# Kernel optimization log

Measured on AMD Instinct MI355X. Metric: run time of the kernel, lower is better.

The kernel has to match this reference:

```python
import jax, jax.numpy as jnp
import numpy as np
from functools import partial

D_MODEL = 1024
D_STATE = 128
D_INNER = 2 * D_MODEL          # 2048
HEADS = D_MODEL                # dt width == d_model -> one dt per head
HEAD_DIM = D_INNER // HEADS    # 2
KERNEL = 4
PROJ_OUT = 2 * D_INNER + 2 * D_STATE + D_MODEL  # 5376


def setup_inputs() -> dict:
    key = jax.random.key(0)
    ks = jax.random.split(key, 8)
    B, L = 2, 2048
    u = jax.random.normal(ks[0], (B, L, D_MODEL), dtype=jnp.float32)
    W_in = jax.random.normal(ks[1], (D_MODEL, PROJ_OUT), dtype=jnp.float32) * 0.02
    conv_w = jax.random.normal(ks[2], (D_INNER, 1, KERNEL), dtype=jnp.float32) * 0.2
    conv_b = jnp.zeros((D_INNER,), dtype=jnp.float32)
    W_out = jax.random.normal(ks[3], (D_INNER, D_MODEL), dtype=jnp.float32) * 0.02
    ln_g = jnp.ones((D_MODEL,), dtype=jnp.float32)
    ln_b = jnp.zeros((D_MODEL,), dtype=jnp.float32)
    A_log = jnp.log(jax.random.uniform(ks[4], (HEADS,), minval=1.0, maxval=16.0)).astype(jnp.float32)
    return {"u": u, "W_in": W_in, "conv_w": conv_w, "conv_b": conv_b,
            "W_out": W_out, "ln_g": ln_g, "ln_b": ln_b, "A_log": A_log}


def _layernorm(x, g, b, eps=1e-5):
    mu = jnp.mean(x, axis=-1, keepdims=True)
    var = jnp.var(x, axis=-1, keepdims=True)
    return (x - mu) * jax.lax.rsqrt(var + eps) * g + b


def _mamba2_forward(u, W_in, conv_w, conv_b, W_out, ln_g, ln_b, A_log):
    B, L, _ = u.shape
    xn = _layernorm(u, ln_g, ln_b)
    zxbcdt = xn @ W_in                                   # (B, L, PROJ_OUT)
    x, z, Bc, Cc, dt = jnp.split(
        zxbcdt, [D_INNER, 2 * D_INNER, 2 * D_INNER + D_STATE,
                 2 * D_INNER + 2 * D_STATE], axis=-1)
    # causal depthwise conv over time (pad left KERNEL-1)
    xc = jnp.transpose(x, (0, 2, 1))                     # (B, C, L)
    xc = jnp.pad(xc, ((0, 0), (0, 0), (KERNEL - 1, 0)))
    xc = jax.lax.conv_general_dilated(
        xc, conv_w, window_strides=(1,), padding='VALID',
        dimension_numbers=('NCH', 'OIH', 'NCH'),
        feature_group_count=D_INNER) + conv_b[None, :, None]
    x = jax.nn.silu(jnp.transpose(xc, (0, 2, 1)))        # (B, L, d_inner)

    dt = jax.nn.softplus(dt)                             # (B, L, H)
    A = -jnp.exp(A_log)                                  # (H,)
    decay = jnp.exp(dt * A)                              # (B, L, H)
    xh = x.reshape(B, L, HEADS, HEAD_DIM)                # (B, L, H, P)

    # time-major for scan
    def step(h, inp):
        dec_t, dt_t, x_t, B_t, C_t = inp                 # (B,H),(B,H),(B,H,P),(B,N),(B,N)
        h = dec_t[..., None, None] * h + \
            (dt_t[..., None] * x_t)[..., None] * B_t[:, None, None, :]
        y_t = jnp.einsum('bhpn,bn->bhp', h, C_t)
        return h, y_t

    tm = lambda a: jnp.swapaxes(a, 0, 1)
    h0 = jnp.zeros((B, HEADS, HEAD_DIM, D_STATE), dtype=u.dtype)
    _, ys = jax.lax.scan(step, h0, (tm(decay), tm(dt), tm(xh), tm(Bc), tm(Cc)))
    y = jnp.swapaxes(ys, 0, 1).reshape(B, L, D_INNER)    # (B, L, d_inner)

    y = y * jax.nn.silu(z)
    return u + y @ W_out                                 # residual


def reference(u, W_in, conv_w, conv_b, W_out, ln_g, ln_b, A_log):
    return _mamba2_forward(u, W_in, conv_w, conv_b, W_out, ln_g, ln_b, A_log)
```

## Files before the change

kernel.cpp:

```cpp
#include <hip/hip_runtime.h>
#include <hip/hip_bf16.h>
#include <stdint.h>

typedef __bf16 bf16_t;
typedef bf16_t bf16x8 __attribute__((ext_vector_type(8)));
typedef bf16_t bf16x4 __attribute__((ext_vector_type(4)));
typedef bf16_t bf16x2 __attribute__((ext_vector_type(2)));
typedef float  f32x4  __attribute__((ext_vector_type(4)));

#define D_MODEL 1024
#define D_STATE 128
#define D_INNER 2048
#define HEADS   1024
#define PROJ    5376
#define LSEQ    2048
#define BATCH   2
#define NROW    (BATCH*LSEQ)
#define QCH     64
#define NC      (LSEQ/QCH)

#define OFF_X   0
#define OFF_Z   2048
#define OFF_B   4096
#define OFF_C   4224
#define OFF_DT  4352

#define LOG2E 1.44269504088896340736f

typedef __attribute__((address_space(1))) void void_as1;
typedef __attribute__((address_space(3))) void void_as3;

__device__ __forceinline__ void gload_lds16(const void* g, void* l) {
  __builtin_amdgcn_global_load_lds((void_as1*)(uintptr_t)g,
                                   (void_as3*)(uint32_t)(uintptr_t)l,
                                   16, 0, 0);
}

__device__ __forceinline__ float siluf(float v) { return v / (1.f + expf(-v)); }

__device__ __forceinline__ float exp2_fast(float x) {
  float r;
  asm("v_exp_f32 %0, %1" : "=v"(r) : "v"(x));
  return r;
}

__device__ __forceinline__ float rdlane(float v, int l) {
  return __int_as_float(__builtin_amdgcn_readlane(__float_as_int(v), l));
}

template<int CTRL, int RM>
__device__ __forceinline__ float dpp_add(float x) {
  int s = __builtin_amdgcn_update_dpp(0, __float_as_int(x), CTRL, RM, 0xf, true);
  return x + __int_as_float(s);
}

__global__ __launch_bounds__(256) void transpose_kernel(const float* __restrict__ src,
                                                        bf16_t* __restrict__ dst,
                                                        int R, int C) {
  __shared__ float tile[32][33];
  int c0 = blockIdx.x * 32, r0 = blockIdx.y * 32;
  int tx = threadIdx.x, ty = threadIdx.y;
  #pragma unroll
  for (int i = ty; i < 32; i += 8)
    tile[i][tx] = src[(size_t)(r0 + i) * C + c0 + tx];
  __syncthreads();
  #pragma unroll
  for (int i = ty; i < 32; i += 8)
    dst[(size_t)(c0 + i) * R + r0 + tx] = (bf16_t)tile[tx][i];
}

__global__ __launch_bounds__(256) void ln_kernel(const float* __restrict__ u,
                                                 const float* __restrict__ g,
                                                 const float* __restrict__ bb,
                                                 bf16_t* __restrict__ xn) {
  int row = blockIdx.x;
  int t = threadIdx.x;
  float4 v = ((const float4*)(u + (size_t)row * D_MODEL))[t];
  float s  = v.x + v.y + v.z + v.w;
  float s2 = v.x*v.x + v.y*v.y + v.z*v.z + v.w*v.w;
  #pragma unroll
  for (int m = 1; m < 64; m <<= 1) { s += __shfl_xor(s, m, 64); s2 += __shfl_xor(s2, m, 64); }
  __shared__ float ws[8];
  int wv = t >> 6, lane = t & 63;
  if (lane == 0) { ws[wv] = s; ws[4 + wv] = s2; }
  __syncthreads();
  s  = ws[0] + ws[1] + ws[2] + ws[3];
  s2 = ws[4] + ws[5] + ws[6] + ws[7];
  float mean = s * (1.f / D_MODEL);
  float var  = s2 * (1.f / D_MODEL) - mean * mean;
  float rstd = rsqrtf(var + 1e-5f);
  float4 gv = ((const float4*)g)[t];
  float4 bv = ((const float4*)bb)[t];
  bf16x4 o;
  o[0] = (bf16_t)((v.x - mean) * rstd * gv.x + bv.x);
  o[1] = (bf16_t)((v.y - mean) * rstd * gv.y + bv.y);
  o[2] = (bf16_t)((v.z - mean) * rstd * gv.z + bv.z);
  o[3] = (bf16_t)((v.w - mean) * rstd * gv.w + bv.w);
  *(bf16x4*)(xn + (size_t)row * D_MODEL + t * 4) = o;
}

template<typename CT>
__global__ __launch_bounds__(256) void gemm_bt(const bf16_t* __restrict__ A,
                                               const bf16_t* __restrict__ BT,
                                               CT* __restrict__ C,
                                               int M, int N, int K,
                                               const float* __restrict__ resid,
                                               int tilesPerBatch,
                                               long long sA, long long sB, long long sC) {
  __shared__ bf16_t lA[128 * 32];
  __shared__ bf16_t lB[128 * 32];
  int bat = blockIdx.x / tilesPerBatch;
  int tl  = blockIdx.x % tilesPerBatch;
  A += (size_t)bat * sA; BT += (size_t)bat * sB; C += (size_t)bat * sC;
  int ntile = N >> 7;
  int tm = tl / ntile, tn = tl % ntile;
  int m0 = tm << 7, n0 = tn << 7;
  int t = threadIdx.x;
  int wv = t >> 6, lane = t & 63;
  int wm = (wv >> 1) << 6, wn = (wv & 1) << 6;
  int l15 = lane & 15, l4 = lane >> 4;

  f32x4 acc[4][4];
  #pragma unroll
  for (int i = 0; i < 4; ++i)
    #pragma unroll
    for (int j = 0; j < 4; ++j) acc[i][j] = (f32x4){0.f, 0.f, 0.f, 0.f};

  int sr = t >> 2;
  int sk = (t & 3) * 8;
  const bf16_t* ga  = A  + (size_t)(m0 + sr) * K + sk;
  const bf16_t* ga2 = ga + (size_t)64 * K;
  const bf16_t* gb  = BT + (size_t)(n0 + sr) * K + sk;
  const bf16_t* gb2 = gb + (size_t)64 * K;
  bf16_t* la  = lA + t * 8;
  bf16_t* la2 = la + 2048;
  bf16_t* lb  = lB + t * 8;
  bf16_t* lb2 = lb + 2048;

  const bf16_t* raBase = lA + (wm + l15) * 32 + l4 * 8;
  const bf16_t* rbBase = lB + (wn + l15) * 32 + l4 * 8;

  for (int k0 = 0; k0 < K; k0 += 32) {
    gload_lds16(ga, la);  gload_lds16(ga2, la2);
    gload_lds16(gb, lb);  gload_lds16(gb2, lb2);
    ga += 32; ga2 += 32; gb += 32; gb2 += 32;
    __syncthreads();
    bf16x8 af[4], bq[4];
    #pragma unroll
    for (int f = 0; f < 4; ++f) {
      af[f] = *(const bf16x8*)(raBase + f * 512);
      bq[f] = *(const bf16x8*)(rbBase + f * 512);
    }
    #pragma unroll
    for (int i = 0; i < 4; ++i)
      #pragma unroll
      for (int j = 0; j < 4; ++j)
        acc[i][j] = __builtin_amdgcn_mfma_f32_16x16x32_bf16(af[i], bq[j], acc[i][j], 0, 0, 0);
    __syncthreads();
  }

  #pragma unroll
  for (int i = 0; i < 4; ++i) {
    int row = m0 + wm + i * 16 + l4 * 4;
    #pragma unroll
    for (int j = 0; j < 4; ++j) {
      int col = n0 + wn + j * 16 + l15;
      #pragma unroll
      for (int r = 0; r < 4; ++r) {
        size_t idx = (size_t)(row + r) * N + col;
        float v = acc[i][j][r];
        if (resid) v += resid[idx];
        C[idx] = (CT)v;
      }
    }
  }
}

__global__ __launch_bounds__(256) void prep_kernel(const bf16_t* __restrict__ zxb,
                                                   const float* __restrict__ conv_w,
                                                   const float* __restrict__ conv_b,
                                                   const float* __restrict__ A_log,
                                                   float* __restrict__ dta,
                                                   bf16_t* __restrict__ dtx) {
  int idx = blockIdx.x * 256 + threadIdx.x;
  int h  = idx & (HEADS - 1);
  int bt = idx >> 10;
  int t  = bt & (LSEQ - 1);
  float draw = (float)zxb[(size_t)bt * PROJ + OFF_DT + h];
  float dt = (draw > 20.f) ? draw : log1pf(expf(draw));
  float Ah = -expf(A_log[h]);
  dta[idx] = dt * Ah;
  float4 w0 = *(const float4*)(conv_w + 8 * h);
  float4 w1 = *(const float4*)(conv_w + 8 * h + 4);
  float2 cb = *(const float2*)(conv_b + 2 * h);
  float acc0 = cb.x, acc1 = cb.y;
  float w0a[4] = {w0.x, w0.y, w0.z, w0.w};
  float w1a[4] = {w1.x, w1.y, w1.z, w1.w};
  #pragma unroll
  for (int k = 0; k < 4; ++k) {
    int tt = t - 3 + k;
    if (tt >= 0) {
      bf16x2 xv = *(const bf16x2*)(zxb + (size_t)(bt - 3 + k) * PROJ + OFF_X + 2 * h);
      acc0 = fmaf((float)xv[0], w0a[k], acc0);
      acc1 = fmaf((float)xv[1], w1a[k], acc1);
    }
  }
  float xs0 = siluf(acc0), xs1 = siluf(acc1);
  bf16x2 o; o[0] = (bf16_t)(dt * xs0); o[1] = (bf16_t)(dt * xs1);
  *(bf16x2*)(dtx + 2 * (size_t)idx) = o;
}

__global__ __launch_bounds__(256) void kg_kernel(const bf16_t* __restrict__ zxb,
                                                 float* __restrict__ GT,
                                                 bf16_t* __restrict__ BTc) {
  __shared__ bf16_t lB[QCH * 128];
  __shared__ bf16_t lC[QCH * 128];
  int bc = blockIdx.x;
  int b = bc / NC, c = bc % NC;
  int t = threadIdx.x;
  size_t rowbase = ((size_t)b * LSEQ + c * QCH);
  #pragma unroll
  for (int p = 0; p < 4; ++p) {
    int row = p * 16 + (t >> 4);
    int eo  = (t & 15) * 8;
    gload_lds16(zxb + (rowbase + row) * PROJ + OFF_B + eo, lB + p * 2048 + t * 8);
    gload_lds16(zxb + (rowbase + row) * PROJ + OFF_C + eo, lC + p * 2048 + t * 8);
  }
  __syncthreads();
  int wv = t >> 6, lane = t & 63;
  int l15 = lane & 15, l4 = lane >> 4;
  f32x4 acc[4];
  #pragma unroll
  for (int i = 0; i < 4; ++i) acc[i] = (f32x4){0.f, 0.f, 0.f, 0.f};
  #pragma unroll
  for (int ks = 0; ks < 4; ++ks) {
    bf16x8 af = *(const bf16x8*)(lB + (16 * wv + l15) * 128 + ks * 32 + l4 * 8);
    #pragma unroll
    for (int it = 0; it < 4; ++it) {
      bf16x8 bq = *(const bf16x8*)(lC + (16 * it + l15) * 128 + ks * 32 + l4 * 8);
      acc[it] = __builtin_amdgcn_mfma_f32_16x16x32_bf16(af, bq, acc[it], 0, 0, 0);
    }
  }
  float* gout = GT + (size_t)bc * 4096;
  #pragma unroll
  for (int it = 0; it < 4; ++it) {
    int col = it * 16 + l15;
    #pragma unroll
    for (int r = 0; r < 4; ++r) {
      int j = 16 * wv + l4 * 4 + r;
      gout[j * 64 + col] = acc[it][r];
    }
  }
  bf16_t* bto = BTc + (size_t)bc * (128 * QCH);
  int n = t >> 1, j0 = (t & 1) * 32;
  #pragma unroll
  for (int jj = 0; jj < 32; ++jj)
    bto[n * QCH + j0 + jj] = lB[(j0 + jj) * 128 + n];
}

__global__ __launch_bounds__(512) void local_kernel(const float* __restrict__ GT,
                                                    const float* __restrict__ dta,
                                                    const bf16_t* __restrict__ dtx,
                                                    float* __restrict__ y,
                                                    bf16_t* __restrict__ S,
                                                    bf16_t* __restrict__ cdb,
                                                    float* __restrict__ Dch) {
  __shared__ float sp[4096];
  __shared__ float sy[QCH * 17];
  int t = threadIdx.x;
  int wv = t >> 6, l = t & 63;
  int hg = blockIdx.x & 127;
  int c  = (blockIdx.x >> 7) & (NC - 1);
  int b  = blockIdx.x >> 12;
  int bc = b * NC + c;
  int h  = hg * 8 + wv;

  {
    const float* gsrc = GT + (size_t)bc * 4096 + t * 8;
    float4 a = *(const float4*)gsrc;
    float4 bq = *(const float4*)(gsrc + 4);
    int j  = t >> 3;
    int i0 = (t & 7) * 8;
    float va[8] = {a.x, a.y, a.z, a.w, bq.x, bq.y, bq.z, bq.w};
    float* dstb = sp + (j >> 1) * 128 + (j & 1);
    #pragma unroll
    for (int k = 0; k < 8; ++k) {
      int i = i0 + k;
      dstb[i * 2] = (j <= i) ? va[k] : 0.f;
    }
  }

  int tIdx = c * QCH + l;
  size_t bt = (size_t)b * LSEQ + tIdx;
  float dtal = dta[bt * HEADS + h];
  bf16x2 vvb = *(const bf16x2*)(dtx + bt * D_INNER + 2 * h);
  float v0 = (float)vvb[0], v1 = (float)vvb[1];

  float ca = dtal;
  ca = dpp_add<0x111, 0xf>(ca);
  ca = dpp_add<0x112, 0xf>(ca);
  ca = dpp_add<0x114, 0xf>(ca);
  ca = dpp_add<0x118, 0xf>(ca);
  ca = dpp_add<0x142, 0xa>(ca);
  ca = dpp_add<0x143, 0xc>(ca);
  float ca2 = ca * LOG2E;

  float cdl = exp2_fast(ca2);
  cdb[((size_t)b * HEADS + h) * LSEQ + tIdx] = (bf16_t)cdl;
  float calast2 = rdlane(ca2, 63);
  float sc = exp2_fast(calast2 - ca2);
  bf16_t* srow = S + ((size_t)bc * D_INNER + 2 * h) * QCH + l;
  srow[0]   = (bf16_t)(sc * v0);
  srow[QCH] = (bf16_t)(sc * v1);
  if (l == 63) Dch[((size_t)b * HEADS + h) * NC + c] = cdl;
  __syncthreads();

  float y0 = 0.f, y1 = 0.f;
  const float* spb = sp + l * 2;
  #pragma unroll
  for (int j2 = 0; j2 < 32; ++j2) {
    float2 g2 = *(const float2*)(spb + j2 * 128);
    {
      float cj2 = rdlane(ca2, 2 * j2);
      float sv0 = rdlane(v0, 2 * j2);
      float sv1 = rdlane(v1, 2 * j2);
      float e = exp2_fast(fminf(ca2 - cj2, 0.f));
      float gg = e * g2.x;
      y0 = fmaf(gg, sv0, y0);
      y1 = fmaf(gg, sv1, y1);
    }
    {
      float cj2 = rdlane(ca2, 2 * j2 + 1);
      float sv0 = rdlane(v0, 2 * j2 + 1);
      float sv1 = rdlane(v1, 2 * j2 + 1);
      float e = exp2_fast(fminf(ca2 - cj2, 0.f));
      float gg = e * g2.y;
      y0 = fmaf(gg, sv0, y0);
      y1 = fmaf(gg, sv1, y1);
    }
  }
  sy[l * 17 + wv * 2]     = y0;
  sy[l * 17 + wv * 2 + 1] = y1;
  __syncthreads();
  int rowt = t >> 3, cc = (t & 7) * 2;
  float2 o = make_float2(sy[rowt * 17 + cc], sy[rowt * 17 + cc + 1]);
  *(float2*)(y + ((size_t)b * LSEQ + c * QCH + rowt) * D_INNER + hg * 16 + cc) = o;
}

__global__ __launch_bounds__(256) void state_kernel(bf16_t* __restrict__ Hst,
                                                    const float* __restrict__ Dch) {
  int g = blockIdx.x * 256 + threadIdx.x;
  int nq = g & 31;
  int hp = (g >> 5) & (D_INNER - 1);
  int b  = g >> 16;
  int h  = hp >> 1;
  const float* Dp = Dch + ((size_t)b * HEADS + h) * NC;
  float4 cur = make_float4(0.f, 0.f, 0.f, 0.f);
  for (int c = 0; c < NC; ++c) {
    size_t idx = (((size_t)(b * NC + c) * D_INNER) + hp) * D_STATE + nq * 4;
    bf16x4 old = *(bf16x4*)(Hst + idx);
    bf16x4 w;
    w[0] = (bf16_t)cur.x; w[1] = (bf16_t)cur.y; w[2] = (bf16_t)cur.z; w[3] = (bf16_t)cur.w;
    *(bf16x4*)(Hst + idx) = w;
    float d = Dp[c];
    cur.x = fmaf(d, cur.x, (float)old[0]);
    cur.y = fmaf(d, cur.y, (float)old[1]);
    cur.z = fmaf(d, cur.z, (float)old[2]);
    cur.w = fmaf(d, cur.w, (float)old[3]);
  }
}

__global__ __launch_bounds__(256) void ycross_kernel(const bf16_t* __restrict__ zxb,
                                                     const bf16_t* __restrict__ Hst,
                                                     const bf16_t* __restrict__ cdb,
                                                     float* __restrict__ y) {
  __shared__ bf16_t lA[QCH * 32];
  __shared__ bf16_t lB[256 * 32];
  int nt = blockIdx.x & 7;
  int c  = (blockIdx.x >> 3) & (NC - 1);
  int b  = blockIdx.x >> 8;
  int bc = b * NC + c;
  int n0 = nt * 256;
  int t = threadIdx.x;
  int wv = t >> 6, lane = t & 63;
  int l15 = lane & 15, l4 = lane >> 4;
  size_t rowbase = (size_t)b * LSEQ + c * QCH;

  f32x4 acc[4][4];
  #pragma unroll
  for (int i = 0; i < 4; ++i)
    #pragma unroll
    for (int j = 0; j < 4; ++j) acc[i][j] = (f32x4){0.f, 0.f, 0.f, 0.f};

  int sr = t >> 2, sk = (t & 3) * 8;
  for (int ks = 0; ks < 4; ++ks) {
    int k0 = ks * 32;
    gload_lds16(zxb + (rowbase + sr) * PROJ + OFF_C + k0 + sk, lA + t * 8);
    #pragma unroll
    for (int p = 0; p < 4; ++p)
      gload_lds16(Hst + ((size_t)bc * D_INNER + n0 + p * 64 + sr) * D_STATE + k0 + sk,
                  lB + p * 2048 + t * 8);
    __syncthreads();
    #pragma unroll
    for (int i = 0; i < 4; ++i) {
      bf16x8 af = *(const bf16x8*)(lA + (i * 16 + l15) * 32 + l4 * 8);
      #pragma unroll
      for (int j = 0; j < 4; ++j) {
        bf16x8 bq = *(const bf16x8*)(lB + (wv * 64 + j * 16 + l15) * 32 + l4 * 8);
        acc[i][j] = __builtin_amdgcn_mfma_f32_16x16x32_bf16(af, bq, acc[i][j], 0, 0, 0);
      }
    }
    __syncthreads();
  }

  #pragma unroll
  for (int i = 0; i < 4; ++i) {
    int row = i * 16 + l4 * 4;
    #pragma unroll
    for (int j = 0; j < 4; ++j) {
      int col = n0 + wv * 64 + j * 16 + l15;
      int h = col >> 1;
      bf16x4 cd4 = *(const bf16x4*)(cdb + ((size_t)b * HEADS + h) * LSEQ + c * QCH + row);
      #pragma unroll
      for (int r = 0; r < 4; ++r) {
        size_t idx = (rowbase + row + r) * D_INNER + col;
        y[idx] += (float)cd4[r] * acc[i][j][r];
      }
    }
  }
}

__global__ __launch_bounds__(256) void gate_kernel(const float* __restrict__ y,
                                                   const bf16_t* __restrict__ zxb,
                                                   bf16_t* __restrict__ yg) {
  int tid = blockIdx.x * 256 + threadIdx.x;
  int row = tid >> 9;
  int c0  = (tid & 511) * 4;
  float4 yv = *(const float4*)(y + (size_t)row * D_INNER + c0);
  bf16x4 zv = *(const bf16x4*)(zxb + (size_t)row * PROJ + OFF_Z + c0);
  bf16x4 o;
  o[0] = (bf16_t)(yv.x * siluf((float)zv[0]));
  o[1] = (bf16_t)(yv.y * siluf((float)zv[1]));
  o[2] = (bf16_t)(yv.z * siluf((float)zv[2]));
  o[3] = (bf16_t)(yv.w * siluf((float)zv[3]));
  *(bf16x4*)(yg + (size_t)row * D_INNER + c0) = o;
}

extern "C" void kernel_launch(void* const* d_in, const int* in_sizes, int n_in,
                              void* d_out, int out_size, void* d_ws, size_t ws_size,
                              hipStream_t stream) {
  const float* u      = (const float*)d_in[0];
  const float* W_in   = (const float*)d_in[1];
  const float* conv_w = (const float*)d_in[2];
  const float* conv_b = (const float*)d_in[3];
  const float* W_out  = (const float*)d_in[4];
  const float* ln_g   = (const float*)d_in[5];
  const float* ln_b   = (const float*)d_in[6];
  const float* A_log  = (const float*)d_in[7];
  float* out = (float*)d_out;

  char* ws = (char*)d_ws;
  bf16_t* W_inT  = (bf16_t*)ws;  ws += (size_t)PROJ * D_MODEL * 2;
  bf16_t* W_outT = (bf16_t*)ws;  ws += (size_t)D_MODEL * D_INNER * 2;
  bf16_t* xn     = (bf16_t*)ws;  ws += (size_t)NROW * D_MODEL * 2;
  bf16_t* zxb    = (bf16_t*)ws;  ws += (size_t)NROW * PROJ * 2;
  float*  dta    = (float*)ws;   ws += (size_t)NROW * HEADS * 4;
  bf16_t* dtx    = (bf16_t*)ws;  ws += (size_t)NROW * D_INNER * 2;
  float*  yy     = (float*)ws;   ws += (size_t)NROW * D_INNER * 4;
  bf16_t* yg     = (bf16_t*)ws;  ws += (size_t)NROW * D_INNER * 2;
  float*  GT     = (float*)ws;   ws += (size_t)BATCH * NC * 4096 * 4;
  bf16_t* BTc    = (bf16_t*)ws;  ws += (size_t)BATCH * NC * 128 * QCH * 2;
  bf16_t* S      = (bf16_t*)ws;  ws += (size_t)BATCH * NC * D_INNER * QCH * 2;
  bf16_t* cdb    = (bf16_t*)ws;  ws += (size_t)BATCH * HEADS * LSEQ * 2;
  float*  Dch    = (float*)ws;   ws += (size_t)BATCH * HEADS * NC * 4;
  bf16_t* Hst    = (bf16_t*)ws;  ws += (size_t)BATCH * NC * D_INNER * D_STATE * 2;

  dim3 tb(32, 8);
  transpose_kernel<<<dim3(PROJ / 32, D_MODEL / 32), tb, 0, stream>>>(W_in, W_inT, D_MODEL, PROJ);
  transpose_kernel<<<dim3(D_MODEL / 32, D_INNER / 32), tb, 0, stream>>>(W_out, W_outT, D_INNER, D_MODEL);
  ln_kernel<<<NROW, 256, 0, stream>>>(u, ln_g, ln_b, xn);
  gemm_bt<bf16_t><<<(NROW / 128) * (PROJ / 128), 256, 0, stream>>>(
      xn, W_inT, zxb, NROW, PROJ, D_MODEL, nullptr, (NROW / 128) * (PROJ / 128), 0, 0, 0);
  prep_kernel<<<NROW * HEADS / 256, 256, 0, stream>>>(zxb, conv_w, conv_b, A_log, dta, dtx);
  kg_kernel<<<BATCH * NC, 256, 0, stream>>>(zxb, GT, BTc);
  local_kernel<<<BATCH * NC * 128, 512, 0, stream>>>(GT, dta, dtx, yy, S, cdb, Dch);
  gemm_bt<bf16_t><<<BATCH * NC * 16, 256, 0, stream>>>(
      S, BTc, Hst, D_INNER, D_STATE, QCH, nullptr, 16,
      (long long)D_INNER * QCH, (long long)128 * QCH, (long long)D_INNER * D_STATE);
  state_kernel<<<BATCH * D_INNER * 32 / 256, 256, 0, stream>>>(Hst, Dch);
  ycross_kernel<<<BATCH * NC * 8, 256, 0, stream>>>(zxb, Hst, cdb, yy);
  gate_kernel<<<NROW * D_INNER / 4 / 256, 256, 0, stream>>>(yy, zxb, yg);
  gemm_bt<float><<<(NROW / 128) * (D_MODEL / 128), 256, 0, stream>>>(
      yg, W_outT, out, NROW, D_MODEL, D_INNER, u, (NROW / 128) * (D_MODEL / 128), 0, 0, 0);
}
```

Measured before the change: 412.2 us.

## Add pipelined 8-wave input-projection GEMM and double-buffer generic GEMM

```diff
diff --git a/kernel.cpp b/kernel.cpp
--- a/kernel.cpp
+++ b/kernel.cpp
@@ -99,6 +99,120 @@
   *(bf16x4*)(xn + (size_t)row * D_MODEL + t * 4) = o;
 }
 
+#define G1_NT 16
+#define MFMA_BF16(a,b,c) __builtin_amdgcn_mfma_f32_16x16x32_bf16(a,b,c,0,0,0)
+
+__global__ __launch_bounds__(512, 2) void gemm1_8ph(const bf16_t* __restrict__ A,
+                                                    const bf16_t* __restrict__ BT,
+                                                    bf16_t* __restrict__ C) {
+  __shared__ __align__(16) char smem[98304];
+  int bid = blockIdx.x;
+  int s8  = (bid & 7) * 84 + (bid >> 3);
+  int tm = s8 / 21, tn = s8 % 21;
+  int m0 = tm << 7, n0 = tn << 8;
+  int tid = threadIdx.x;
+  int wid = tid >> 6, lane = tid & 63;
+  int wm = wid >> 2, wn = wid & 3;
+  int l15 = lane & 15, l4 = lane >> 4;
+
+  const bf16_t* Ab = A  + (size_t)m0 * 1024;
+  const bf16_t* Bb = BT + (size_t)n0 * 1024;
+  int rowA = tid >> 3;
+  int gcol = ((tid & 7) ^ (rowA & 7)) * 8;
+
+  int sw0 = (l4 * 16) ^ ((l15 & 7) << 4);
+  int sw1 = sw0 ^ 64;
+  int ar0 = (wm * 32 + l15) * 128;
+  int ar1 = ar0 + 2048;
+  int br0 = (wn * 32 + l15) * 128;
+  int br1 = br0 + 2048;
+
+  f32x4 acc[2][2][2][2];
+  #pragma unroll
+  for (int a = 0; a < 2; ++a)
+    #pragma unroll
+    for (int b = 0; b < 2; ++b)
+      #pragma unroll
+      for (int c = 0; c < 2; ++c)
+        #pragma unroll
+        for (int d = 0; d < 2; ++d) acc[a][b][c][d] = (f32x4){0.f,0.f,0.f,0.f};
+
+#define STAGE_A(half, t) do { \
+    const bf16_t* _s = Ab + ((size_t)((half)*64 + rowA) * 1024) + (t)*64 + gcol; \
+    gload_lds16(_s, smem + ((t)&1)*49152 + (half)*8192 + tid*16); \
+  } while(0)
+#define STAGE_B(half, t) do { \
+    const bf16_t* _s = Bb + ((size_t)((half)*128 + rowA) * 1024) + (t)*64 + gcol; \
+    char* _d = smem + ((t)&1)*49152 + 16384 + (half)*16384 + tid*16; \
+    gload_lds16(_s, _d); \
+    gload_lds16(_s + 64*1024, _d + 8192); \
+  } while(0)
+
+#define PHASE(qm, qn, dd, STMT_STAGE, STMT_VM) do { \
+    const char* pa = smem + (dd)*49152 + (qm)*8192; \
+    const char* pb = smem + (dd)*49152 + 16384 + (qn)*16384; \
+    bf16x8 a00 = *(const bf16x8*)(pa + ar0 + sw0); \
+    bf16x8 a01 = *(const bf16x8*)(pa + ar0 + sw1); \
+    bf16x8 a10 = *(const bf16x8*)(pa + ar1 + sw0); \
+    bf16x8 a11 = *(const bf16x8*)(pa + ar1 + sw1); \
+    bf16x8 b00 = *(const bf16x8*)(pb + br0 + sw0); \
+    bf16x8 b01 = *(const bf16x8*)(pb + br0 + sw1); \
+    bf16x8 b10 = *(const bf16x8*)(pb + br1 + sw0); \
+    bf16x8 b11 = *(const bf16x8*)(pb + br1 + sw1); \
+    STMT_STAGE; \
+    __builtin_amdgcn_s_barrier(); \
+    asm volatile("s_waitcnt lgkmcnt(0)" ::: "memory"); \
+    __builtin_amdgcn_sched_barrier(0); \
+    __builtin_amdgcn_s_setprio(1); \
+    acc[qm][qn][0][0] = MFMA_BF16(a00, b00, acc[qm][qn][0][0]); \
+    acc[qm][qn][0][1] = MFMA_BF16(a00, b10, acc[qm][qn][0][1]); \
+    acc[qm][qn][1][0] = MFMA_BF16(a10, b00, acc[qm][qn][1][0]); \
+    acc[qm][qn][1][1] = MFMA_BF16(a10, b10, acc[qm][qn][1][1]); \
+    acc[qm][qn][0][0] = MFMA_BF16(a01, b01, acc[qm][qn][0][0]); \
+    acc[qm][qn][0][1] = MFMA_BF16(a01, b11, acc[qm][qn][0][1]); \
+    acc[qm][qn][1][0] = MFMA_BF16(a11, b01, acc[qm][qn][1][0]); \
+    acc[qm][qn][1][1] = MFMA_BF16(a11, b11, acc[qm][qn][1][1]); \
+    __builtin_amdgcn_s_setprio(0); \
+    __builtin_amdgcn_sched_barrier(0); \
+    STMT_VM; \
+    __builtin_amdgcn_s_barrier(); \
+  } while(0)
+
+  STAGE_A(0, 0); STAGE_B(0, 0); STAGE_B(1, 0); STAGE_A(1, 0);
+  STAGE_A(0, 1); STAGE_B(0, 1);
+  asm volatile("s_waitcnt vmcnt(3)" ::: "memory");
+  __builtin_amdgcn_s_barrier();
+
+  for (int t = 0; t < G1_NT; ++t) {
+    int dd = t & 1;
+    PHASE(0, 0, dd, { if (t + 1 < G1_NT) STAGE_B(1, t + 1); }, {});
+    PHASE(0, 1, dd, { if (t + 1 < G1_NT) STAGE_A(1, t + 1); }, {});
+    PHASE(1, 0, dd, { if (t + 2 < G1_NT) STAGE_A(0, t + 2); }, {});
+    PHASE(1, 1, dd, { if (t + 2 < G1_NT) STAGE_B(0, t + 2); },
+          { if (t <= G1_NT - 3) asm volatile("s_waitcnt vmcnt(3)" ::: "memory");
+            else                asm volatile("s_waitcnt vmcnt(0)" ::: "memory"); });
+  }
+
+  #pragma unroll
+  for (int qm = 0; qm < 2; ++qm)
+    #pragma unroll
+    for (int qn = 0; qn < 2; ++qn)
+      #pragma unroll
+      for (int mf = 0; mf < 2; ++mf)
+        #pragma unroll
+        for (int nf = 0; nf < 2; ++nf) {
+          int row = m0 + qm * 64 + wm * 32 + mf * 16 + l4 * 4;
+          int col = n0 + qn * 128 + wn * 32 + nf * 16 + l15;
+          f32x4 v = acc[qm][qn][mf][nf];
+          #pragma unroll
+          for (int r = 0; r < 4; ++r)
+            C[(size_t)(row + r) * PROJ + col] = (bf16_t)v[r];
+        }
+#undef STAGE_A
+#undef STAGE_B
+#undef PHASE
+}
+
 template<typename CT>
 __global__ __launch_bounds__(256) void gemm_bt(const bf16_t* __restrict__ A,
                                                const bf16_t* __restrict__ BT,
@@ -107,8 +221,8 @@
                                                const float* __restrict__ resid,
                                                int tilesPerBatch,
                                                long long sA, long long sB, long long sC) {
-  __shared__ bf16_t lA[128 * 32];
-  __shared__ bf16_t lB[128 * 32];
+  __shared__ __align__(16) bf16_t lA[2][128 * 32];
+  __shared__ __align__(16) bf16_t lB[2][128 * 32];
   int bat = blockIdx.x / tilesPerBatch;
   int tl  = blockIdx.x % tilesPerBatch;
   A += (size_t)bat * sA; BT += (size_t)bat * sB; C += (size_t)bat * sC;
@@ -132,32 +246,42 @@
   const bf16_t* ga2 = ga + (size_t)64 * K;
   const bf16_t* gb  = BT + (size_t)(n0 + sr) * K + sk;
   const bf16_t* gb2 = gb + (size_t)64 * K;
-  bf16_t* la  = lA + t * 8;
-  bf16_t* la2 = la + 2048;
-  bf16_t* lb  = lB + t * 8;
-  bf16_t* lb2 = lb + 2048;
-
-  const bf16_t* raBase = lA + (wm + l15) * 32 + l4 * 8;
-  const bf16_t* rbBase = lB + (wn + l15) * 32 + l4 * 8;
-
+
+  int raOff = (wm + l15) * 64 + l4 * 16;
+  int rbOff = (wn + l15) * 64 + l4 * 16;
+
+#define ST2(dd) do { \
+    char* _da = (char*)lA + (dd) * 8192 + t * 16; \
+    char* _db = (char*)lB + (dd) * 8192 + t * 16; \
+    gload_lds16(ga, _da);  gload_lds16(ga2, _da + 4096); \
+    gload_lds16(gb, _db);  gload_lds16(gb2, _db + 4096); \
+    ga += 32; ga2 += 32; gb += 32; gb2 += 32; \
+  } while(0)
+
+  ST2(0);
+  asm volatile("s_waitcnt vmcnt(0)" ::: "memory");
+  __builtin_amdgcn_s_barrier();
+
+  int cur = 0;
   for (int k0 = 0; k0 < K; k0 += 32) {
-    gload_lds16(ga, la);  gload_lds16(ga2, la2);
-    gload_lds16(gb, lb);  gload_lds16(gb2, lb2);
-    ga += 32; ga2 += 32; gb += 32; gb2 += 32;
-    __syncthreads();
+    if (k0 + 32 < K) ST2(cur ^ 1);
     bf16x8 af[4], bq[4];
     #pragma unroll
     for (int f = 0; f < 4; ++f) {
-      af[f] = *(const bf16x8*)(raBase + f * 512);
-      bq[f] = *(const bf16x8*)(rbBase + f * 512);
+      af[f] = *(const bf16x8*)((const char*)lA + cur * 8192 + raOff + f * 1024);
+      bq[f] = *(const bf16x8*)((const char*)lB + cur * 8192 + rbOff + f * 1024);
     }
     #pragma unroll
     for (int i = 0; i < 4; ++i)
       #pragma unroll
       for (int j = 0; j < 4; ++j)
-        acc[i][j] = __builtin_amdgcn_mfma_f32_16x16x32_bf16(af[i], bq[j], acc[i][j], 0, 0, 0);
-    __syncthreads();
-  }
+        acc[i][j] = MFMA_BF16(af[i], bq[j], acc[i][j]);
+    asm volatile("s_waitcnt lgkmcnt(0)" ::: "memory");
+    asm volatile("s_waitcnt vmcnt(0)" ::: "memory");
+    __builtin_amdgcn_s_barrier();
+    cur ^= 1;
+  }
+#undef ST2
 
   #pragma unroll
   for (int i = 0; i < 4; ++i) {
@@ -479,8 +603,7 @@
   transpose_kernel<<<dim3(PROJ / 32, D_MODEL / 32), tb, 0, stream>>>(W_in, W_inT, D_MODEL, PROJ);
   transpose_kernel<<<dim3(D_MODEL / 32, D_INNER / 32), tb, 0, stream>>>(W_out, W_outT, D_INNER, D_MODEL);
   ln_kernel<<<NROW, 256, 0, stream>>>(u, ln_g, ln_b, xn);
-  gemm_bt<bf16_t><<<(NROW / 128) * (PROJ / 128), 256, 0, stream>>>(
-      xn, W_inT, zxb, NROW, PROJ, D_MODEL, nullptr, (NROW / 128) * (PROJ / 128), 0, 0, 0);
+  gemm1_8ph<<<(NROW / 128) * (PROJ / 256), 512, 0, stream>>>(xn, W_inT, zxb);
   prep_kernel<<<NROW * HEADS / 256, 256, 0, stream>>>(zxb, conv_w, conv_b, A_log, dta, dtx);
   kg_kernel<<<BATCH * NC, 256, 0, stream>>>(zxb, GT, BTc);
   local_kernel<<<BATCH * NC * 128, 512, 0, stream>>>(GT, dta, dtx, yy, S, cdb, Dch);
```

New measurement: 397.7 us. -3.5%, faster.
